# Kernel tuning notes

Measured on AMD Instinct MI355X. Metric: run time of the kernel, lower is better.

The kernel has to match this reference:

```python
import jax, jax.numpy as jnp
import numpy as np

KERNEL_SIZE = 13
SIGMA_MIN, SIGMA_MAX = 0.4, 10.0
BETA, THRESHOLD = 0.95, 1.0


@jax.custom_vjp
def spike(x):
    # Heaviside forward, snntorch ATan surrogate backward (alpha=2)
    return (x > 0).astype(x.dtype)

def _spike_fwd(x):
    return spike(x), x

def _spike_bwd(x, g):
    return (g / (1.0 + (jnp.pi * x) ** 2),)

spike.defvjp(_spike_fwd, _spike_bwd)


def setup_inputs() -> dict:
    key = jax.random.key(0)
    k1, k2 = jax.random.split(key)
    B, C, T = 32, 224, 2048
    inp = jax.random.normal(k1, (B, 1, C, T), dtype=jnp.float32)
    linear_w = jax.random.normal(k2, (1, C), dtype=jnp.float32) * (1.0 / np.sqrt(C))
    return {"inp": inp, "linear_w": linear_w}


def _forward(inp, linear_w):
    x = inp[:, 0]  # [B, C, T]
    B, C, T = x.shape
    sigma_mean = 0.5 * (SIGMA_MIN + SIGMA_MAX)
    # adaptive sigma per (batch, time): Linear over channel axis, no bias
    w = sigma_mean + jnp.einsum('bct,c->bt', x, linear_w[0]) * (SIGMA_MAX - SIGMA_MIN)
    w = jnp.clip(w, SIGMA_MIN, SIGMA_MAX)  # [B, T]

    half = KERNEL_SIZE // 2
    r = jnp.linspace(-half, half, KERNEL_SIZE)
    r_all = jnp.linspace(-half * 10, half * 10, KERNEL_SIZE * 10)
    sig = w[..., None]  # [B, T, 1]
    kern = jnp.exp(-0.5 * (r / sig) ** 2)                       # [B, T, K]
    norm = jnp.exp(-0.5 * (r_all / sig) ** 2).sum(-1, keepdims=True)
    kern = kern / norm                                          # normalized over fine grid

    # adaptive gaussian smoothing along the CHANNEL axis (per timestep kernel)
    xt = jnp.transpose(x, (0, 2, 1))                            # [B, T, C]
    padded = jnp.pad(xt, ((0, 0), (0, 0), (half, half)))        # zero pad channels
    x_mean = sum(padded[:, :, k:k + C] * kern[:, :, k:k + 1]
                 for k in range(KERNEL_SIZE))                   # [B, T, C]
    x_mean = jnp.transpose(x_mean, (0, 2, 1))                   # [B, C, T]

    I = x - jax.nn.relu(x - x_mean)                             # soft min(x, x_mean)

    # Leaky-integrate-and-fire over time (snntorch Leaky, reset-by-subtract)
    def step(mem, I_t):
        reset = jax.lax.stop_gradient((mem > THRESHOLD).astype(I_t.dtype))
        mem = BETA * mem + I_t - reset * THRESHOLD
        spk = spike(mem - THRESHOLD)
        return mem, spk

    I_seq = jnp.transpose(I, (2, 0, 1))                         # [T, B, C]
    _, spk = jax.lax.scan(step, jnp.zeros((B, C), I.dtype), I_seq)
    spk = jnp.transpose(spk, (1, 2, 0))                         # [B, C, T]
    return spk[:, None]                                         # [B, 1, C, T]


def reference(inp, linear_w):
    return _forward(inp, linear_w)
```

## Files before the change

### kernel.cpp

```cpp
#include <hip/hip_runtime.h>
#include <math.h>

#define BB 32
#define CCH 224
#define TTT 2048
#define TPB 64
#define NT  (TTT/TPB)
#define CG  28
#define NCG (CCH/CG)
#define ROWS 40
#define XROW 68
#define IROW 29

__global__ __launch_bounds__(256) void kw(
    const float* __restrict__ x, const float* __restrict__ lw,
    double* __restrict__ kernG)
{
    const int b = blockIdx.y;
    const int t = blockIdx.x * 256 + threadIdx.x;
    const float* xb = x + (((size_t)b * CCH) << 11) + t;

    double p0 = 0, p1 = 0, p2 = 0, p3 = 0;
    #pragma unroll 8
    for (int i = 0; i < 56; ++i) {
        p0 += (double)xb[(size_t)i << 11]         * (double)lw[i];
        p1 += (double)xb[(size_t)(i + 56) << 11]  * (double)lw[i + 56];
        p2 += (double)xb[(size_t)(i + 112) << 11] * (double)lw[i + 112];
        p3 += (double)xb[(size_t)(i + 168) << 11] * (double)lw[i + 168];
    }
    double acc = (p0 + p1) + (p2 + p3);

    double w = 5.2 + acc * 9.6;
    w = fmin(fmax(w, 0.4), 10.0);
    double iw2 = 1.0 / (w * w);

    const double s = 120.0 / 129.0;
    double G  = exp(-0.125 * s * s * iw2);
    double G2 = G * G, G4 = G2 * G2, G8 = G4 * G4;
    double term = G, cmul = G8, norm = G;
    for (int u = 1; u <= 64; ++u) { term *= cmul; cmul *= G8; norm += term; }
    norm *= 2.0;

    double P = exp(-0.5 * iw2), P2 = P * P;
    double a = 1.0, bm = P, inv = 1.0 / norm;
    double* kr = kernG + (size_t)(b * TTT + t) * 7;
    kr[0] = inv;
    #pragma unroll
    for (int d = 1; d <= 6; ++d) {
        a *= bm; bm *= P2;
        kr[d] = a * inv;
    }
}

__global__ __launch_bounds__(192) void kf(
    const float* __restrict__ x, const double* __restrict__ kernG,
    float* __restrict__ out)
{
    __shared__ __align__(16) float xs[2][ROWS][XROW];
    __shared__ double kd[2][TPB][7];
    __shared__ double Is[2][TPB][IROW];
    __shared__ unsigned long long bitsb[2][CG];

    const int b   = blockIdx.y;
    const int cgi = blockIdx.x;
    const int c0  = cgi * CG;
    const int tid = threadIdx.x;
    const int ctid = tid - 64;

    const float*  xbase = x + (((size_t)(b * CCH)) << 11);
    const double* kbase = kernG + (size_t)(b * TTT) * 7;
    float* obase = out + (((size_t)(b * CCH + c0)) << 11);

    double mem = 0.0;
    bool   r   = false;

    if (tid >= 64) {
        #pragma unroll
        for (int i2 = 0; i2 < 5; ++i2) {
            int e = ctid + i2 * 128;
            int rr = e >> 4, q = e & 15;
            int cr = c0 - 6 + rr;
            float4 v = make_float4(0.f, 0.f, 0.f, 0.f);
            if (cr >= 0 && cr < CCH)
                v = *(const float4*)(xbase + ((size_t)cr << 11) + 4 * q);
            *(float4*)&xs[0][rr][4 * q] = v;
        }
        if (ctid < TPB) {
            const double* kp = kbase + (size_t)ctid * 7;
            #pragma unroll
            for (int i2 = 0; i2 < 7; ++i2) kd[0][ctid][i2] = kp[i2];
        }
    }
    __syncthreads();

    for (int k = 0; k <= NT + 1; ++k) {
        if (tid >= 64) {
            const int buf = k & 1, nbuf = (k + 1) & 1;
            float4 rv[5]; double kv[7];
            const bool st = (k + 1 <= NT - 1);
            if (st) {
                const int gt0 = (k + 1) * TPB;
                #pragma unroll
                for (int i2 = 0; i2 < 5; ++i2) {
                    int e = ctid + i2 * 128;
                    int rr = e >> 4, q = e & 15;
                    int cr = c0 - 6 + rr;
                    rv[i2] = make_float4(0.f, 0.f, 0.f, 0.f);
                    if (cr >= 0 && cr < CCH)
                        rv[i2] = *(const float4*)(xbase + ((size_t)cr << 11) + gt0 + 4 * q);
                }
                if (ctid < TPB) {
                    const double* kp = kbase + (size_t)(gt0 + ctid) * 7;
                    #pragma unroll
                    for (int i2 = 0; i2 < 7; ++i2) kv[i2] = kp[i2];
                }
            }
            if (k <= NT - 1) {
                const int t  = ctid & 63;
                const int ch = ctid >> 6;
                const int cb = 14 * ch;
                double kk7[7];
                #pragma unroll
                for (int i2 = 0; i2 < 7; ++i2) kk7[i2] = kd[buf][t][i2];
                float xv[13];
                #pragma unroll
                for (int i2 = 0; i2 < 13; ++i2) xv[i2] = xs[buf][cb + i2][t];
                #pragma unroll
                for (int c = 0; c < 14; ++c) {
                    double acc = 0.0;
                    #pragma unroll
                    for (int kk2 = 0; kk2 < 13; ++kk2) {
                        int d = kk2 < 6 ? 6 - kk2 : kk2 - 6;
                        acc = fma((double)xv[(c + kk2) % 13], kk7[d], acc);
                    }
                    double xvv = (double)xv[(c + 6) % 13];
                    double dd  = xvv - acc;
                    Is[buf][t][cb + c] = xvv - (dd > 0.0 ? dd : 0.0);
                    if (c < 13) xv[c % 13] = xs[buf][cb + c + 13][t];
                }
            }
            if (k >= 2) {
                const int j = k - 2, jb = j & 1;
                const int t0o = j * TPB;
                #pragma unroll
                for (int i2 = 0; i2 < 4; ++i2) {
                    int e = ctid + i2 * 128;
                    if (e < 448) {
                        int c = e >> 4, q = e & 15;
                        unsigned long long bits = bitsb[jb][c] >> (4 * q);
                        float4 v;
                        v.x = (bits & 1ull) ? 1.0f : 0.0f;
                        v.y = (bits & 2ull) ? 1.0f : 0.0f;
                        v.z = (bits & 4ull) ? 1.0f : 0.0f;
                        v.w = (bits & 8ull) ? 1.0f : 0.0f;
                        *(float4*)(obase + ((size_t)c << 11) + t0o + 4 * q) = v;
                    }
                }
            }
            if (st) {
                #pragma unroll
                for (int i2 = 0; i2 < 5; ++i2) {
                    int e = ctid + i2 * 128;
                    int rr = e >> 4, q = e & 15;
                    *(float4*)&xs[nbuf][rr][4 * q] = rv[i2];
                }
                if (ctid < TPB) {
                    #pragma unroll
                    for (int i2 = 0; i2 < 7; ++i2) kd[nbuf][ctid][i2] = kv[i2];
                }
            }
        } else {
            if (k >= 1 && k <= NT) {
                const int p = (k - 1) & 1;
                const int c = tid;
                if (c < CG) {
                    unsigned long long bits = 0ull;
                    double va[8], vb[8];
                    #pragma unroll
                    for (int j2 = 0; j2 < 8; ++j2) va[j2] = Is[p][j2][c];
                    #pragma unroll
                    for (int g = 0; g < 64; g += 16) {
                        #pragma unroll
                        for (int j2 = 0; j2 < 8; ++j2) vb[j2] = Is[p][g + 8 + j2][c];
                        #pragma unroll
                        for (int j2 = 0; j2 < 8; ++j2) {
                            double a2 = va[j2];
                            double cm = a2 - 1.0;
                            double m1 = fma(0.95, mem, a2);
                            double m2 = fma(0.95, mem, cm);
                            mem = r ? m2 : m1;
                            r = mem > 1.0;
                            bits |= (unsigned long long)(r ? 1 : 0) << (g + j2);
                        }
                        if (g + 16 < 64) {
                            #pragma unroll
                            for (int j2 = 0; j2 < 8; ++j2) va[j2] = Is[p][g + 16 + j2][c];
                        }
                        #pragma unroll
                        for (int j2 = 0; j2 < 8; ++j2) {
                            double a2 = vb[j2];
                            double cm = a2 - 1.0;
                            double m1 = fma(0.95, mem, a2);
                            double m2 = fma(0.95, mem, cm);
                            mem = r ? m2 : m1;
                            r = mem > 1.0;
                            bits |= (unsigned long long)(r ? 1 : 0) << (g + 8 + j2);
                        }
                    }
                    bitsb[p][c] = bits;
                }
            }
        }
        __syncthreads();
    }
}

extern "C" void kernel_launch(void* const* d_in, const int* in_sizes, int n_in,
                              void* d_out, int out_size, void* d_ws, size_t ws_size,
                              hipStream_t stream)
{
    const float* x  = (const float*)d_in[0];
    const float* lw = (const float*)d_in[1];
    float* out = (float*)d_out;

    double* kernG = (double*)d_ws;

    kw<<<dim3(TTT / 256, BB), 256, 0, stream>>>(x, lw, kernG);
    kf<<<dim3(NCG, BB), 192, 0, stream>>>(x, kernG, out);
}
```

Before: 152.3 us.

## Halve channel group size in LIF kernel and split kw reduction across warps

The filter/LIF kernel now processes 14 channels per block instead of 28, doubling the grid to 16x32 blocks so more CUs are busy during the serial time scan. The price is a larger halo overhead (26 rows loaded for 14 channels instead of 40 for 28). The sigma kernel splits the 224-channel dot product across four 64-thread groups and reduces through shared memory. This gives four times as many blocks and less serial work per thread, while only one wave runs the expensive norm computation.

```diff
diff --git a/kernel.cpp b/kernel.cpp
--- a/kernel.cpp
+++ b/kernel.cpp
@@ -6,49 +6,55 @@
 #define TTT 2048
 #define TPB 64
 #define NT  (TTT/TPB)
-#define CG  28
+#define CG  14
 #define NCG (CCH/CG)
-#define ROWS 40
+#define ROWS 26
 #define XROW 68
-#define IROW 29
+#define IROW 15
 
 __global__ __launch_bounds__(256) void kw(
     const float* __restrict__ x, const float* __restrict__ lw,
     double* __restrict__ kernG)
 {
-    const int b = blockIdx.y;
-    const int t = blockIdx.x * 256 + threadIdx.x;
-    const float* xb = x + (((size_t)b * CCH) << 11) + t;
-
-    double p0 = 0, p1 = 0, p2 = 0, p3 = 0;
+    __shared__ double sp[4][64];
+    const int b  = blockIdx.y;
+    const int tl = threadIdx.x & 63;
+    const int q  = threadIdx.x >> 6;
+    const int t  = blockIdx.x * 64 + tl;
+
+    const float* xb  = x + (((size_t)(b * CCH + 56 * q)) << 11) + t;
+    const float* lwq = lw + 56 * q;
+
+    double p = 0.0;
     #pragma unroll 8
-    for (int i = 0; i < 56; ++i) {
-        p0 += (double)xb[(size_t)i << 11]         * (double)lw[i];
-        p1 += (double)xb[(size_t)(i + 56) << 11]  * (double)lw[i + 56];
-        p2 += (double)xb[(size_t)(i + 112) << 11] * (double)lw[i + 112];
-        p3 += (double)xb[(size_t)(i + 168) << 11] * (double)lw[i + 168];
-    }
-    double acc = (p0 + p1) + (p2 + p3);
-
-    double w = 5.2 + acc * 9.6;
-    w = fmin(fmax(w, 0.4), 10.0);
-    double iw2 = 1.0 / (w * w);
-
-    const double s = 120.0 / 129.0;
-    double G  = exp(-0.125 * s * s * iw2);
-    double G2 = G * G, G4 = G2 * G2, G8 = G4 * G4;
-    double term = G, cmul = G8, norm = G;
-    for (int u = 1; u <= 64; ++u) { term *= cmul; cmul *= G8; norm += term; }
-    norm *= 2.0;
-
-    double P = exp(-0.5 * iw2), P2 = P * P;
-    double a = 1.0, bm = P, inv = 1.0 / norm;
-    double* kr = kernG + (size_t)(b * TTT + t) * 7;
-    kr[0] = inv;
-    #pragma unroll
-    for (int d = 1; d <= 6; ++d) {
-        a *= bm; bm *= P2;
-        kr[d] = a * inv;
+    for (int i = 0; i < 56; ++i)
+        p += (double)xb[(size_t)i << 11] * (double)lwq[i];
+    sp[q][tl] = p;
+    __syncthreads();
+
+    if (threadIdx.x < 64) {
+        double acc = (sp[0][tl] + sp[1][tl]) + (sp[2][tl] + sp[3][tl]);
+
+        double w = 5.2 + acc * 9.6;
+        w = fmin(fmax(w, 0.4), 10.0);
+        double iw2 = 1.0 / (w * w);
+
+        const double s = 120.0 / 129.0;
+        double G  = exp(-0.125 * s * s * iw2);
+        double G2 = G * G, G4 = G2 * G2, G8 = G4 * G4;
+        double term = G, cmul = G8, norm = G;
+        for (int u = 1; u <= 64; ++u) { term *= cmul; cmul *= G8; norm += term; }
+        norm *= 2.0;
+
+        double P = exp(-0.5 * iw2), P2 = P * P;
+        double a = 1.0, bm = P, inv = 1.0 / norm;
+        double* kr = kernG + (size_t)(b * TTT + t) * 7;
+        kr[0] = inv;
+        #pragma unroll
+        for (int d = 1; d <= 6; ++d) {
+            a *= bm; bm *= P2;
+            kr[d] = a * inv;
+        }
     }
 }
 
@@ -76,14 +82,16 @@
 
     if (tid >= 64) {
         #pragma unroll
-        for (int i2 = 0; i2 < 5; ++i2) {
+        for (int i2 = 0; i2 < 4; ++i2) {
             int e = ctid + i2 * 128;
-            int rr = e >> 4, q = e & 15;
-            int cr = c0 - 6 + rr;
-            float4 v = make_float4(0.f, 0.f, 0.f, 0.f);
-            if (cr >= 0 && cr < CCH)
-                v = *(const float4*)(xbase + ((size_t)cr << 11) + 4 * q);
-            *(float4*)&xs[0][rr][4 * q] = v;
+            if (e < ROWS * 16) {
+                int rr = e >> 4, qq = e & 15;
+                int cr = c0 - 6 + rr;
+                float4 v = make_float4(0.f, 0.f, 0.f, 0.f);
+                if (cr >= 0 && cr < CCH)
+                    v = *(const float4*)(xbase + ((size_t)cr << 11) + 4 * qq);
+                *(float4*)&xs[0][rr][4 * qq] = v;
+            }
         }
         if (ctid < TPB) {
             const double* kp = kbase + (size_t)ctid * 7;
@@ -96,18 +104,20 @@
     for (int k = 0; k <= NT + 1; ++k) {
         if (tid >= 64) {
             const int buf = k & 1, nbuf = (k + 1) & 1;
-            float4 rv[5]; double kv[7];
+            float4 rv[4]; double kv[7];
             const bool st = (k + 1 <= NT - 1);
             if (st) {
                 const int gt0 = (k + 1) * TPB;
                 #pragma unroll
-                for (int i2 = 0; i2 < 5; ++i2) {
+                for (int i2 = 0; i2 < 4; ++i2) {
                     int e = ctid + i2 * 128;
-                    int rr = e >> 4, q = e & 15;
-                    int cr = c0 - 6 + rr;
-                    rv[i2] = make_float4(0.f, 0.f, 0.f, 0.f);
-                    if (cr >= 0 && cr < CCH)
-                        rv[i2] = *(const float4*)(xbase + ((size_t)cr << 11) + gt0 + 4 * q);
+                    if (e < ROWS * 16) {
+                        int rr = e >> 4, qq = e & 15;
+                        int cr = c0 - 6 + rr;
+                        rv[i2] = make_float4(0.f, 0.f, 0.f, 0.f);
+                        if (cr >= 0 && cr < CCH)
+                            rv[i2] = *(const float4*)(xbase + ((size_t)cr << 11) + gt0 + 4 * qq);
+                    }
                 }
                 if (ctid < TPB) {
                     const double* kp = kbase + (size_t)(gt0 + ctid) * 7;
@@ -118,7 +128,7 @@
             if (k <= NT - 1) {
                 const int t  = ctid & 63;
                 const int ch = ctid >> 6;
-                const int cb = 14 * ch;
+                const int cb = 7 * ch;
                 double kk7[7];
                 #pragma unroll
                 for (int i2 = 0; i2 < 7; ++i2) kk7[i2] = kd[buf][t][i2];
@@ -126,7 +136,7 @@
                 #pragma unroll
                 for (int i2 = 0; i2 < 13; ++i2) xv[i2] = xs[buf][cb + i2][t];
                 #pragma unroll
-                for (int c = 0; c < 14; ++c) {
+                for (int c = 0; c < 7; ++c) {
                     double acc = 0.0;
                     #pragma unroll
                     for (int kk2 = 0; kk2 < 13; ++kk2) {
@@ -136,33 +146,35 @@
                     double xvv = (double)xv[(c + 6) % 13];
                     double dd  = xvv - acc;
                     Is[buf][t][cb + c] = xvv - (dd > 0.0 ? dd : 0.0);
-                    if (c < 13) xv[c % 13] = xs[buf][cb + c + 13][t];
+                    if (c < 6) xv[c % 13] = xs[buf][cb + c + 13][t];
                 }
             }
             if (k >= 2) {
                 const int j = k - 2, jb = j & 1;
                 const int t0o = j * TPB;
                 #pragma unroll
-                for (int i2 = 0; i2 < 4; ++i2) {
+                for (int i2 = 0; i2 < 2; ++i2) {
                     int e = ctid + i2 * 128;
-                    if (e < 448) {
-                        int c = e >> 4, q = e & 15;
-                        unsigned long long bits = bitsb[jb][c] >> (4 * q);
+                    if (e < CG * 16) {
+                        int c = e >> 4, qq = e & 15;
+                        unsigned long long bits = bitsb[jb][c] >> (4 * qq);
                         float4 v;
                         v.x = (bits & 1ull) ? 1.0f : 0.0f;
                         v.y = (bits & 2ull) ? 1.0f : 0.0f;
                         v.z = (bits & 4ull) ? 1.0f : 0.0f;
                         v.w = (bits & 8ull) ? 1.0f : 0.0f;
-                        *(float4*)(obase + ((size_t)c << 11) + t0o + 4 * q) = v;
+                        *(float4*)(obase + ((size_t)c << 11) + t0o + 4 * qq) = v;
                     }
                 }
             }
             if (st) {
                 #pragma unroll
-                for (int i2 = 0; i2 < 5; ++i2) {
+                for (int i2 = 0; i2 < 4; ++i2) {
                     int e = ctid + i2 * 128;
-                    int rr = e >> 4, q = e & 15;
-                    *(float4*)&xs[nbuf][rr][4 * q] = rv[i2];
+                    if (e < ROWS * 16) {
+                        int rr = e >> 4, qq = e & 15;
+                        *(float4*)&xs[nbuf][rr][4 * qq] = rv[i2];
+                    }
                 }
                 if (ctid < TPB) {
                     #pragma unroll
@@ -225,6 +237,6 @@
 
     double* kernG = (double*)d_ws;
 
-    kw<<<dim3(TTT / 256, BB), 256, 0, stream>>>(x, lw, kernG);
+    kw<<<dim3(TTT / 64, BB), 256, 0, stream>>>(x, lw, kernG);
     kf<<<dim3(NCG, BB), 192, 0, stream>>>(x, kernG, out);
 }
```

New measurement: 157.4 us. 1.03x slower.
